# Kernel optimization log

Hardware: AMD Instinct MI355X
Metric: run time of the kernel (lower is better)

The kernel has to match this reference:

```python
import jax, jax.numpy as jnp
import numpy as np

ASSIGN_RATIO = 0.1  # hard-coded inside coarsen_graph in the original
EPS_CUT = 1e-7
EPS_NORM = 1e-12  # torch F.normalize eps


def _normalize_batch_adj(adj):
    # adj: [B, N, N]
    n = adj.shape[1]
    A = adj + jnp.eye(n, dtype=adj.dtype)
    deg_inv_sqrt = jnp.clip(A.sum(-1), 1.0, None) ** -0.5  # [B, N]
    newA = deg_inv_sqrt[..., :, None] * A * deg_inv_sqrt[..., None, :]
    row_mask = (adj.sum(-1) > 0).astype(adj.dtype)  # [B, N]
    return row_mask[..., :, None] * newA


def setup_inputs():
    key = jax.random.key(0)
    k0, k1, k2, k3, k4 = jax.random.split(key, 5)
    B, N, D, T = 512, 128, 256, 512
    concept_hidden = jax.random.normal(k0, (B, N, D), jnp.float32)
    adj = jax.random.uniform(k1, (B, N, N), jnp.float32)
    head = jax.random.randint(k2, (B, T), 0, N)
    lin_w = jax.random.normal(k3, (1, D), jnp.float32) / np.sqrt(D).astype(np.float32)
    bias = jax.random.normal(k4, (1,), jnp.float32)
    return {"concept_hidden": concept_hidden, "adj": adj, "head": head,
            "lin_w": lin_w, "bias": bias}


def reference(concept_hidden, adj, head, lin_w, bias):
    # concept_hidden: [B, N, D], adj: [B, N, N], head: [B, T] node indices
    x = concept_hidden
    B, N, D = x.shape

    out = x @ lin_w.T                      # [B, N, 1]  self.lin(x)
    norm_adj = _normalize_batch_adj(adj)   # [B, N, N]
    out = norm_adj @ out + bias            # [B, N, 1]
    alpha = jax.nn.sigmoid(out ** 2)[..., 0]  # [B, N]

    # batch_num_nodes[i] = len(set(head[i]))  -> count unique via sort
    hs = jnp.sort(head, axis=-1)
    n_uniq = 1 + (hs[:, 1:] != hs[:, :-1]).sum(-1)  # [B]

    # per-sample k = ceil(n * 0.1) + 1 (only when n > 1); cut = k-th largest alpha
    k = jnp.ceil(n_uniq.astype(jnp.float32) * ASSIGN_RATIO).astype(jnp.int32) + 1
    a_desc = jnp.sort(alpha, axis=-1)[:, ::-1]       # descending
    idx = jnp.clip(k - 1, 0, N - 1)
    cut = jnp.take_along_axis(a_desc, idx[:, None], axis=-1)[:, 0]
    cut = jnp.where(n_uniq > 1, cut, jnp.zeros_like(cut))  # [B]

    cut_alpha = jax.nn.relu(alpha + EPS_CUT - cut[:, None])  # [B, N]

    # S = norm_adj * cut_alpha broadcast over rows, then L1-normalize rows
    S = norm_adj * cut_alpha[:, None, :]
    S = S / jnp.clip(jnp.abs(S).sum(-1, keepdims=True), EPS_NORM, None)

    St = jnp.swapaxes(S, 1, 2)             # [B, N, N]
    embedding_tensor = St @ x              # S^T x   [B, N, D]
    new_adj = (St @ adj) @ S               # S^T A S [B, N, N]
    return embedding_tensor, new_adj
```

## Files before the change

kernel.cpp:

```cpp
#include <hip/hip_runtime.h>

#define Bsz 512
#define Nn  128
#define Dd  256
#define Tt  512

typedef __attribute__((ext_vector_type(8))) short short8;
typedef __attribute__((ext_vector_type(4))) float f32x4;

__device__ __forceinline__ ushort f2bf(float f) {
    union { float f; unsigned u; } v; v.f = f;
    unsigned r = v.u + 0x7fffu + ((v.u >> 16) & 1u);
    return (ushort)(r >> 16);
}
__device__ __forceinline__ unsigned pk2(float a, float b) {
    return (unsigned)f2bf(a) | ((unsigned)f2bf(b) << 16);
}
__device__ __forceinline__ float bf2f(ushort u) {
    union { unsigned u; float f; } v; v.u = (unsigned)u << 16; return v.f;
}

__global__ __launch_bounds__(1024, 8) void mega(
    const float* __restrict__ x, const float* __restrict__ adj,
    const int* __restrict__ head, const float* __restrict__ lin_w,
    const float* __restrict__ bias,
    float* __restrict__ emb, float* __restrict__ nadj)
{
    const int b = blockIdx.x, t = threadIdx.x;
    __shared__ __align__(16) ushort adjB[Nn][136];
    __shared__ __align__(16) ushort STl[Nn][136];
    __shared__ float ttS[Nn], disS[Nn], maskS[Nn], alphaS[Nn], uS[Nn], rowcS[Nn];
    __shared__ float dotL[Nn];
    __shared__ int   flags[Nn];
    __shared__ int   nuniq;
    __shared__ float cutS;

    const float bias0 = bias[0];
    if (t < Nn) flags[t] = 0;
    if (t == 0) { nuniq = 0; cutS = 0.f; }

    int hv = 0;
    if (t < 512) {
        hv = head[(size_t)b * Tt + t];
        const int dr = t >> 2, dh = t & 3;
        const float4* xr = (const float4*)(x + ((size_t)b * Nn + dr) * Dd + dh * 64);
        const float4* wr = (const float4*)(lin_w + dh * 64);
        float p = 0.f;
#pragma unroll
        for (int i = 0; i < 16; ++i) {
            float4 v = xr[i], w4 = wr[i];
            p += v.x * w4.x + v.y * w4.y + v.z * w4.z + v.w * w4.w;
        }
        p += __shfl_xor(p, 1, 64);
        p += __shfl_xor(p, 2, 64);
        if (dh == 0) dotL[dr] = p;
    } else {
        const int t2 = t - 512;
        const float* adjb = adj + (size_t)b * Nn * Nn;
#pragma unroll
        for (int i = 0; i < 8; ++i) {
            int f = t2 + 512 * i;
            int rr = f >> 5, c = (f & 31) * 4;
            float4 v = *(const float4*)&adjb[(size_t)rr * Nn + c];
            uint2 w2; w2.x = pk2(v.x, v.y); w2.y = pk2(v.z, v.w);
            *(uint2*)&adjB[rr][c] = w2;
        }
    }
    __syncthreads();

    if (t < Tt) flags[hv] = 1;

    const int r = t >> 3, seg = t & 7;
    {
        short8 a0 = *(const short8*)&adjB[r][seg * 16];
        short8 a1 = *(const short8*)&adjB[r][seg * 16 + 8];
        float s = 0.f;
#pragma unroll
        for (int j = 0; j < 8; ++j) s += bf2f((ushort)a0[j]) + bf2f((ushort)a1[j]);
        s += __shfl_xor(s, 1, 64);
        s += __shfl_xor(s, 2, 64);
        s += __shfl_xor(s, 4, 64);
        if (seg == 0) {
            maskS[r] = (s > 0.f) ? 1.f : 0.f;
            float dis = 1.f / sqrtf(fmaxf(s + 1.f, 1.f));
            disS[r] = dis;
            ttS[r]  = dis * dotL[r];
        }
    }
    __syncthreads();

    {
        short8 a0 = *(const short8*)&adjB[r][seg * 16];
        short8 a1 = *(const short8*)&adjB[r][seg * 16 + 8];
        float s = 0.f;
#pragma unroll
        for (int j = 0; j < 8; ++j) {
            s += bf2f((ushort)a0[j]) * ttS[seg * 16 + j];
            s += bf2f((ushort)a1[j]) * ttS[seg * 16 + 8 + j];
        }
        s += __shfl_xor(s, 1, 64);
        s += __shfl_xor(s, 2, 64);
        s += __shfl_xor(s, 4, 64);
        if (seg == 0) {
            float o = maskS[r] * disS[r] * (s + ttS[r]) + bias0;
            alphaS[r] = 1.f / (1.f + expf(-o * o));
            atomicAdd(&nuniq, flags[r]);
        }
    }
    __syncthreads();

    if (t < Nn) {
        int nu = nuniq;
        if (nu > 1) {
            int idx = (int)ceilf((float)nu * 0.1f);
            if (idx > Nn - 1) idx = Nn - 1;
            float an = alphaS[t];
            int cg = 0, ce = 0;
            for (int j = 0; j < Nn; ++j) {
                float aj = alphaS[j];
                cg += (aj > an); ce += (aj == an);
            }
            if (cg <= idx && idx < cg + ce) cutS = an;
        }
    }
    __syncthreads();
    if (t < Nn) uS[t] = fmaxf(alphaS[t] + 1e-7f - cutS, 0.f) * disS[t];
    __syncthreads();

    {
        short8 a0 = *(const short8*)&adjB[r][seg * 16];
        short8 a1 = *(const short8*)&adjB[r][seg * 16 + 8];
        float s = 0.f;
#pragma unroll
        for (int j = 0; j < 8; ++j) {
            s += bf2f((ushort)a0[j]) * uS[seg * 16 + j];
            s += bf2f((ushort)a1[j]) * uS[seg * 16 + 8 + j];
        }
        s += __shfl_xor(s, 1, 64);
        s += __shfl_xor(s, 2, 64);
        s += __shfl_xor(s, 4, 64);
        if (seg == 0) {
            float rsum = maskS[r] * disS[r] * (uS[r] + s);
            rowcS[r]   = maskS[r] * disS[r] / fmaxf(rsum, 1e-12f);
        }
    }
    __syncthreads();

    {
        const int m = t & 127, sl = t >> 7, k0 = sl * 16;
        const float um = uS[m];
        float vv[16];
#pragma unroll
        for (int j = 0; j < 16; ++j) {
            int k = k0 + j;
            vv[j] = rowcS[k] * (bf2f(adjB[k][m]) + ((k == m) ? 1.f : 0.f)) * um;
        }
        uint4 p0, p1;
        p0.x = pk2(vv[0],  vv[1]);  p0.y = pk2(vv[2],  vv[3]);
        p0.z = pk2(vv[4],  vv[5]);  p0.w = pk2(vv[6],  vv[7]);
        p1.x = pk2(vv[8],  vv[9]);  p1.y = pk2(vv[10], vv[11]);
        p1.z = pk2(vv[12], vv[13]); p1.w = pk2(vv[14], vv[15]);
        *(uint4*)&STl[m][k0]     = p0;
        *(uint4*)&STl[m][k0 + 8] = p1;
    }
    __syncthreads();

    const int lane = t & 63, w = t >> 6;
    const int l15 = lane & 15, quad = lane >> 4;
    const int mrow  = (w & 7) * 16;
    const int nhalf = (w >> 3) * 64;
    f32x4 acc[4];

#pragma unroll
    for (int nt = 0; nt < 4; ++nt) acc[nt] = (f32x4){0.f, 0.f, 0.f, 0.f};
#pragma unroll
    for (int k0 = 0; k0 < 128; k0 += 32) {
        short8 a0 = *(const short8*)&adjB[mrow + l15][k0 + quad * 8];
#pragma unroll
        for (int nt = 0; nt < 4; ++nt) {
            short8 bf = *(const short8*)&STl[nhalf + nt * 16 + l15][k0 + quad * 8];
            acc[nt] = __builtin_amdgcn_mfma_f32_16x16x32_bf16(a0, bf, acc[nt], 0, 0, 0);
        }
    }
    __syncthreads();

    ushort (*PT)[136] = (ushort(*)[136])&adjB[0][0];
#pragma unroll
    for (int nt = 0; nt < 4; ++nt) {
        int j    = nhalf + nt * 16 + l15;
        int mcol = mrow + quad * 4;
        uint2 w2;
        w2.x = pk2(acc[nt][0], acc[nt][1]);
        w2.y = pk2(acc[nt][2], acc[nt][3]);
        *(uint2*)&PT[j][mcol] = w2;
    }
    __syncthreads();

    const int xrow = t & 127, kq0 = t >> 7;
    float xv0[8], xv1[8];
    {
        const float* xb = x + (size_t)b * Nn * Dd + xrow;
#pragma unroll
        for (int k = 0; k < 8; ++k) xv0[k] = xb[(size_t)(8 * kq0 + k) * Dd];
#pragma unroll
        for (int k = 0; k < 8; ++k) xv1[k] = xb[(size_t)(8 * (kq0 + 8) + k) * Dd];
    }

#pragma unroll
    for (int nt = 0; nt < 4; ++nt) acc[nt] = (f32x4){0.f, 0.f, 0.f, 0.f};
#pragma unroll
    for (int k0 = 0; k0 < 128; k0 += 32) {
        short8 a0 = *(const short8*)&STl[mrow + l15][k0 + quad * 8];
#pragma unroll
        for (int nt = 0; nt < 4; ++nt) {
            short8 bf = *(const short8*)&PT[nhalf + nt * 16 + l15][k0 + quad * 8];
            acc[nt] = __builtin_amdgcn_mfma_f32_16x16x32_bf16(a0, bf, acc[nt], 0, 0, 0);
        }
    }
#pragma unroll
    for (int nt = 0; nt < 4; ++nt)
#pragma unroll
        for (int rr2 = 0; rr2 < 4; ++rr2) {
            int row = mrow + quad * 4 + rr2;
            int col = nhalf + nt * 16 + l15;
            nadj[((size_t)b * Nn + row) * Nn + col] = acc[nt][rr2];
        }
    __syncthreads();

    uint (*xTp)[68] = (uint(*)[68])&adjB[0][0];
    const int dcb = (w >> 3) * 64;

    {
        uint4 q;
        q.x = pk2(xv0[0], xv0[1]); q.y = pk2(xv0[2], xv0[3]);
        q.z = pk2(xv0[4], xv0[5]); q.w = pk2(xv0[6], xv0[7]);
        *(uint4*)&xTp[xrow][4 * kq0] = q;
        q.x = pk2(xv1[0], xv1[1]); q.y = pk2(xv1[2], xv1[3]);
        q.z = pk2(xv1[4], xv1[5]); q.w = pk2(xv1[6], xv1[7]);
        *(uint4*)&xTp[xrow][4 * (kq0 + 8)] = q;
    }
    __syncthreads();

    {
        const float* xb = x + (size_t)b * Nn * Dd + 128 + xrow;
#pragma unroll
        for (int k = 0; k < 8; ++k) xv0[k] = xb[(size_t)(8 * kq0 + k) * Dd];
#pragma unroll
        for (int k = 0; k < 8; ++k) xv1[k] = xb[(size_t)(8 * (kq0 + 8) + k) * Dd];
    }

    f32x4 accE[4];
#pragma unroll
    for (int nt = 0; nt < 4; ++nt) accE[nt] = (f32x4){0.f, 0.f, 0.f, 0.f};
#pragma unroll
    for (int ks = 0; ks < 4; ++ks) {
        short8 aE = *(const short8*)&STl[mrow + l15][ks * 32 + quad * 8];
#pragma unroll
        for (int nt = 0; nt < 4; ++nt) {
            short8 bf = *(const short8*)&xTp[dcb + nt * 16 + l15][ks * 16 + quad * 4];
            accE[nt] = __builtin_amdgcn_mfma_f32_16x16x32_bf16(aE, bf, accE[nt], 0, 0, 0);
        }
    }
#pragma unroll
    for (int nt = 0; nt < 4; ++nt)
#pragma unroll
        for (int rr2 = 0; rr2 < 4; ++rr2) {
            int row = mrow + quad * 4 + rr2;
            int col = dcb + nt * 16 + l15;
            emb[((size_t)b * Nn + row) * Dd + col] = accE[nt][rr2];
        }
    __syncthreads();

    {
        uint4 q;
        q.x = pk2(xv0[0], xv0[1]); q.y = pk2(xv0[2], xv0[3]);
        q.z = pk2(xv0[4], xv0[5]); q.w = pk2(xv0[6], xv0[7]);
        *(uint4*)&xTp[xrow][4 * kq0] = q;
        q.x = pk2(xv1[0], xv1[1]); q.y = pk2(xv1[2], xv1[3]);
        q.z = pk2(xv1[4], xv1[5]); q.w = pk2(xv1[6], xv1[7]);
        *(uint4*)&xTp[xrow][4 * (kq0 + 8)] = q;
    }
    __syncthreads();

#pragma unroll
    for (int nt = 0; nt < 4; ++nt) accE[nt] = (f32x4){0.f, 0.f, 0.f, 0.f};
#pragma unroll
    for (int ks = 0; ks < 4; ++ks) {
        short8 aE = *(const short8*)&STl[mrow + l15][ks * 32 + quad * 8];
#pragma unroll
        for (int nt = 0; nt < 4; ++nt) {
            short8 bf = *(const short8*)&xTp[dcb + nt * 16 + l15][ks * 16 + quad * 4];
            accE[nt] = __builtin_amdgcn_mfma_f32_16x16x32_bf16(aE, bf, accE[nt], 0, 0, 0);
        }
    }
#pragma unroll
    for (int nt = 0; nt < 4; ++nt)
#pragma unroll
        for (int rr2 = 0; rr2 < 4; ++rr2) {
            int row = mrow + quad * 4 + rr2;
            int col = 128 + dcb + nt * 16 + l15;
            emb[((size_t)b * Nn + row) * Dd + col] = accE[nt][rr2];
        }
}

extern "C" void kernel_launch(void* const* d_in, const int* in_sizes, int n_in,
                              void* d_out, int out_size, void* d_ws, size_t ws_size,
                              hipStream_t stream)
{
    const float* x     = (const float*)d_in[0];
    const float* adj   = (const float*)d_in[1];
    const int*   head  = (const int*)d_in[2];
    const float* lin_w = (const float*)d_in[3];
    const float* bias  = (const float*)d_in[4];

    float* emb  = (float*)d_out;
    float* nadj = emb + (size_t)Bsz * Nn * Dd;

    mega<<<Bsz, 1024, 0, stream>>>(x, adj, head, lin_w, bias, emb, nadj);
}
```

Baseline: 198.9 us.

## Process two batches per block and prefetch next batch's adj and x-projection

Each block now handles two consecutive batch items. While the first item's matmuls run, it prefetches the second item's adjacency into registers and computes the second item's x·w dot products, so those global loads overlap with compute. The cut-value search is also spread across all threads with shuffle reductions instead of 128 threads each scanning serially. The trade-offs are half as many blocks, which means fewer waves and less parallelism across CUs, and higher register pressure from the prefetch buffers.

```diff
diff --git a/kernel.cpp b/kernel.cpp
--- a/kernel.cpp
+++ b/kernel.cpp
@@ -19,288 +19,331 @@
 __device__ __forceinline__ float bf2f(ushort u) {
     union { unsigned u; float f; } v; v.u = (unsigned)u << 16; return v.f;
 }
-
-__global__ __launch_bounds__(1024, 8) void mega(
+__device__ __forceinline__ float dot4(float4 a, float4 b) {
+    return a.x * b.x + a.y * b.y + a.z * b.z + a.w * b.w;
+}
+
+#define RED(p, off) { float v_ = (p); \
+    v_ += __shfl_xor(v_, 1);  v_ += __shfl_xor(v_, 2);  v_ += __shfl_xor(v_, 4); \
+    v_ += __shfl_xor(v_, 8);  v_ += __shfl_xor(v_, 16); v_ += __shfl_xor(v_, 32); \
+    if (lane == 0) dotL[w + (off)] = v_; }
+
+__global__ __launch_bounds__(1024, 4) void mega(
     const float* __restrict__ x, const float* __restrict__ adj,
     const int* __restrict__ head, const float* __restrict__ lin_w,
     const float* __restrict__ bias,
     float* __restrict__ emb, float* __restrict__ nadj)
 {
-    const int b = blockIdx.x, t = threadIdx.x;
+    const int t = threadIdx.x;
     __shared__ __align__(16) ushort adjB[Nn][136];
     __shared__ __align__(16) ushort STl[Nn][136];
-    __shared__ float ttS[Nn], disS[Nn], maskS[Nn], alphaS[Nn], uS[Nn], rowcS[Nn];
-    __shared__ float dotL[Nn];
+    __shared__ float ttS[Nn], disS[Nn], maskS[Nn], alphaS[Nn], uS[Nn], rowcS[Nn], dotL[Nn];
     __shared__ int   flags[Nn];
     __shared__ int   nuniq;
     __shared__ float cutS;
 
     const float bias0 = bias[0];
-    if (t < Nn) flags[t] = 0;
-    if (t == 0) { nuniq = 0; cutS = 0.f; }
-
-    int hv = 0;
-    if (t < 512) {
-        hv = head[(size_t)b * Tt + t];
-        const int dr = t >> 2, dh = t & 3;
-        const float4* xr = (const float4*)(x + ((size_t)b * Nn + dr) * Dd + dh * 64);
-        const float4* wr = (const float4*)(lin_w + dh * 64);
-        float p = 0.f;
-#pragma unroll
-        for (int i = 0; i < 16; ++i) {
-            float4 v = xr[i], w4 = wr[i];
-            p += v.x * w4.x + v.y * w4.y + v.z * w4.z + v.w * w4.w;
-        }
-        p += __shfl_xor(p, 1, 64);
-        p += __shfl_xor(p, 2, 64);
-        if (dh == 0) dotL[dr] = p;
-    } else {
-        const int t2 = t - 512;
-        const float* adjb = adj + (size_t)b * Nn * Nn;
-#pragma unroll
-        for (int i = 0; i < 8; ++i) {
-            int f = t2 + 512 * i;
-            int rr = f >> 5, c = (f & 31) * 4;
-            float4 v = *(const float4*)&adjb[(size_t)rr * Nn + c];
-            uint2 w2; w2.x = pk2(v.x, v.y); w2.y = pk2(v.z, v.w);
-            *(uint2*)&adjB[rr][c] = w2;
-        }
-    }
-    __syncthreads();
-
-    if (t < Tt) flags[hv] = 1;
-
-    const int r = t >> 3, seg = t & 7;
-    {
-        short8 a0 = *(const short8*)&adjB[r][seg * 16];
-        short8 a1 = *(const short8*)&adjB[r][seg * 16 + 8];
-        float s = 0.f;
-#pragma unroll
-        for (int j = 0; j < 8; ++j) s += bf2f((ushort)a0[j]) + bf2f((ushort)a1[j]);
-        s += __shfl_xor(s, 1, 64);
-        s += __shfl_xor(s, 2, 64);
-        s += __shfl_xor(s, 4, 64);
-        if (seg == 0) {
-            maskS[r] = (s > 0.f) ? 1.f : 0.f;
-            float dis = 1.f / sqrtf(fmaxf(s + 1.f, 1.f));
-            disS[r] = dis;
-            ttS[r]  = dis * dotL[r];
-        }
-    }
-    __syncthreads();
-
-    {
-        short8 a0 = *(const short8*)&adjB[r][seg * 16];
-        short8 a1 = *(const short8*)&adjB[r][seg * 16 + 8];
-        float s = 0.f;
-#pragma unroll
-        for (int j = 0; j < 8; ++j) {
-            s += bf2f((ushort)a0[j]) * ttS[seg * 16 + j];
-            s += bf2f((ushort)a1[j]) * ttS[seg * 16 + 8 + j];
-        }
-        s += __shfl_xor(s, 1, 64);
-        s += __shfl_xor(s, 2, 64);
-        s += __shfl_xor(s, 4, 64);
-        if (seg == 0) {
-            float o = maskS[r] * disS[r] * (s + ttS[r]) + bias0;
-            alphaS[r] = 1.f / (1.f + expf(-o * o));
-            atomicAdd(&nuniq, flags[r]);
-        }
-    }
-    __syncthreads();
-
-    if (t < Nn) {
-        int nu = nuniq;
-        if (nu > 1) {
-            int idx = (int)ceilf((float)nu * 0.1f);
-            if (idx > Nn - 1) idx = Nn - 1;
-            float an = alphaS[t];
-            int cg = 0, ce = 0;
-            for (int j = 0; j < Nn; ++j) {
-                float aj = alphaS[j];
-                cg += (aj > an); ce += (aj == an);
-            }
-            if (cg <= idx && idx < cg + ce) cutS = an;
-        }
-    }
-    __syncthreads();
-    if (t < Nn) uS[t] = fmaxf(alphaS[t] + 1e-7f - cutS, 0.f) * disS[t];
-    __syncthreads();
-
-    {
-        short8 a0 = *(const short8*)&adjB[r][seg * 16];
-        short8 a1 = *(const short8*)&adjB[r][seg * 16 + 8];
-        float s = 0.f;
-#pragma unroll
-        for (int j = 0; j < 8; ++j) {
-            s += bf2f((ushort)a0[j]) * uS[seg * 16 + j];
-            s += bf2f((ushort)a1[j]) * uS[seg * 16 + 8 + j];
-        }
-        s += __shfl_xor(s, 1, 64);
-        s += __shfl_xor(s, 2, 64);
-        s += __shfl_xor(s, 4, 64);
-        if (seg == 0) {
-            float rsum = maskS[r] * disS[r] * (uS[r] + s);
-            rowcS[r]   = maskS[r] * disS[r] / fmaxf(rsum, 1e-12f);
-        }
-    }
-    __syncthreads();
-
-    {
-        const int m = t & 127, sl = t >> 7, k0 = sl * 16;
-        const float um = uS[m];
-        float vv[16];
-#pragma unroll
-        for (int j = 0; j < 16; ++j) {
-            int k = k0 + j;
-            vv[j] = rowcS[k] * (bf2f(adjB[k][m]) + ((k == m) ? 1.f : 0.f)) * um;
-        }
-        uint4 p0, p1;
-        p0.x = pk2(vv[0],  vv[1]);  p0.y = pk2(vv[2],  vv[3]);
-        p0.z = pk2(vv[4],  vv[5]);  p0.w = pk2(vv[6],  vv[7]);
-        p1.x = pk2(vv[8],  vv[9]);  p1.y = pk2(vv[10], vv[11]);
-        p1.z = pk2(vv[12], vv[13]); p1.w = pk2(vv[14], vv[15]);
-        *(uint4*)&STl[m][k0]     = p0;
-        *(uint4*)&STl[m][k0 + 8] = p1;
-    }
-    __syncthreads();
-
     const int lane = t & 63, w = t >> 6;
     const int l15 = lane & 15, quad = lane >> 4;
     const int mrow  = (w & 7) * 16;
     const int nhalf = (w >> 3) * 64;
-    f32x4 acc[4];
-
-#pragma unroll
-    for (int nt = 0; nt < 4; ++nt) acc[nt] = (f32x4){0.f, 0.f, 0.f, 0.f};
-#pragma unroll
-    for (int k0 = 0; k0 < 128; k0 += 32) {
-        short8 a0 = *(const short8*)&adjB[mrow + l15][k0 + quad * 8];
+    const int r = t >> 3, seg = t & 7;
+    const int xrow = t & 127, kq0 = t >> 7;
+
+    float4 pf0 = {0,0,0,0}, pf1 = {0,0,0,0}, pf2 = {0,0,0,0}, pf3 = {0,0,0,0};
+
+    for (int it = 0; it < 2; ++it) {
+        const int b = 2 * blockIdx.x + it;
+
+        if (t < Nn) flags[t] = 0;
+        if (t == 0) { nuniq = 0; cutS = 0.f; }
+
+        int hv = 0;
+        if (t < Tt) hv = head[(size_t)b * Tt + t];
+
+        if (it == 0) {
+            if (t < 512) {
+                const int dr = t >> 2, dh = t & 3;
+                const float4* xr = (const float4*)(x + ((size_t)b * Nn + dr) * Dd + dh * 64);
+                const float4* wr = (const float4*)(lin_w + dh * 64);
+                float p = 0.f;
+#pragma unroll
+                for (int i = 0; i < 16; ++i) p += dot4(xr[i], wr[i]);
+                p += __shfl_xor(p, 1);
+                p += __shfl_xor(p, 2);
+                if (dh == 0) dotL[dr] = p;
+            } else {
+                const int t2 = t - 512;
+                const float* adjb = adj + (size_t)b * Nn * Nn;
+#pragma unroll
+                for (int i = 0; i < 8; ++i) {
+                    int f = t2 + 512 * i;
+                    int rr2 = f >> 5, c = (f & 31) * 4;
+                    float4 v = *(const float4*)&adjb[(size_t)rr2 * Nn + c];
+                    uint2 w2; w2.x = pk2(v.x, v.y); w2.y = pk2(v.z, v.w);
+                    *(uint2*)&adjB[rr2][c] = w2;
+                }
+            }
+        } else {
+            float4 v; int f, rr2, c; uint2 w2;
+            v = pf0; f = t;        rr2 = f >> 5; c = (f & 31) * 4; w2.x = pk2(v.x, v.y); w2.y = pk2(v.z, v.w); *(uint2*)&adjB[rr2][c] = w2;
+            v = pf1; f = t + 1024; rr2 = f >> 5; c = (f & 31) * 4; w2.x = pk2(v.x, v.y); w2.y = pk2(v.z, v.w); *(uint2*)&adjB[rr2][c] = w2;
+            v = pf2; f = t + 2048; rr2 = f >> 5; c = (f & 31) * 4; w2.x = pk2(v.x, v.y); w2.y = pk2(v.z, v.w); *(uint2*)&adjB[rr2][c] = w2;
+            v = pf3; f = t + 3072; rr2 = f >> 5; c = (f & 31) * 4; w2.x = pk2(v.x, v.y); w2.y = pk2(v.z, v.w); *(uint2*)&adjB[rr2][c] = w2;
+        }
+        __syncthreads();
+
+        if (t < Tt) flags[hv] = 1;
+
+        {
+            short8 a0 = *(const short8*)&adjB[r][seg * 16];
+            short8 a1 = *(const short8*)&adjB[r][seg * 16 + 8];
+            float s = 0.f;
+#pragma unroll
+            for (int j = 0; j < 8; ++j) s += bf2f((ushort)a0[j]) + bf2f((ushort)a1[j]);
+            s += __shfl_xor(s, 1); s += __shfl_xor(s, 2); s += __shfl_xor(s, 4);
+            if (seg == 0) {
+                maskS[r] = (s > 0.f) ? 1.f : 0.f;
+                float dis = 1.f / sqrtf(fmaxf(s + 1.f, 1.f));
+                disS[r] = dis;
+                ttS[r]  = dis * dotL[r];
+            }
+        }
+        __syncthreads();
+
+        {
+            short8 a0 = *(const short8*)&adjB[r][seg * 16];
+            short8 a1 = *(const short8*)&adjB[r][seg * 16 + 8];
+            float s = 0.f;
+#pragma unroll
+            for (int j = 0; j < 8; ++j) {
+                s += bf2f((ushort)a0[j]) * ttS[seg * 16 + j];
+                s += bf2f((ushort)a1[j]) * ttS[seg * 16 + 8 + j];
+            }
+            s += __shfl_xor(s, 1); s += __shfl_xor(s, 2); s += __shfl_xor(s, 4);
+            if (seg == 0) {
+                float o = maskS[r] * disS[r] * (s + ttS[r]) + bias0;
+                alphaS[r] = 1.f / (1.f + expf(-o * o));
+                atomicAdd(&nuniq, flags[r]);
+            }
+        }
+        __syncthreads();
+
+        {
+            int nu = nuniq;
+            if (nu > 1) {
+                float an = alphaS[r];
+                int cg = 0, ce = 0;
+                const int j0 = seg * 16;
+#pragma unroll
+                for (int j = 0; j < 16; ++j) {
+                    float aj = alphaS[j0 + j];
+                    cg += (aj > an); ce += (aj == an);
+                }
+                cg += __shfl_xor(cg, 1); cg += __shfl_xor(cg, 2); cg += __shfl_xor(cg, 4);
+                ce += __shfl_xor(ce, 1); ce += __shfl_xor(ce, 2); ce += __shfl_xor(ce, 4);
+                if (seg == 0) {
+                    int idx = (int)ceilf((float)nu * 0.1f);
+                    if (idx > Nn - 1) idx = Nn - 1;
+                    if (cg <= idx && idx < cg + ce) cutS = an;
+                }
+            }
+        }
+        __syncthreads();
+        if (t < Nn) uS[t] = fmaxf(alphaS[t] + 1e-7f - cutS, 0.f) * disS[t];
+        __syncthreads();
+
+        {
+            short8 a0 = *(const short8*)&adjB[r][seg * 16];
+            short8 a1 = *(const short8*)&adjB[r][seg * 16 + 8];
+            float s = 0.f;
+#pragma unroll
+            for (int j = 0; j < 8; ++j) {
+                s += bf2f((ushort)a0[j]) * uS[seg * 16 + j];
+                s += bf2f((ushort)a1[j]) * uS[seg * 16 + 8 + j];
+            }
+            s += __shfl_xor(s, 1); s += __shfl_xor(s, 2); s += __shfl_xor(s, 4);
+            if (seg == 0) {
+                float rsum = maskS[r] * disS[r] * (uS[r] + s);
+                rowcS[r]   = maskS[r] * disS[r] / fmaxf(rsum, 1e-12f);
+            }
+        }
+        __syncthreads();
+
+        {
+            const int m = t & 127, sl = t >> 7, k0 = sl * 16;
+            const float um = uS[m];
+            float vv[16];
+#pragma unroll
+            for (int j = 0; j < 16; ++j) {
+                int k = k0 + j;
+                vv[j] = rowcS[k] * (bf2f(adjB[k][m]) + ((k == m) ? 1.f : 0.f)) * um;
+            }
+            uint4 p0, p1;
+            p0.x = pk2(vv[0],  vv[1]);  p0.y = pk2(vv[2],  vv[3]);
+            p0.z = pk2(vv[4],  vv[5]);  p0.w = pk2(vv[6],  vv[7]);
+            p1.x = pk2(vv[8],  vv[9]);  p1.y = pk2(vv[10], vv[11]);
+            p1.z = pk2(vv[12], vv[13]); p1.w = pk2(vv[14], vv[15]);
+            *(uint4*)&STl[m][k0]     = p0;
+            *(uint4*)&STl[m][k0 + 8] = p1;
+        }
+        __syncthreads();
+
+        if (it == 0) {
+            const float4* a1 = (const float4*)(adj + (size_t)(b + 1) * Nn * Nn);
+            pf0 = a1[t]; pf1 = a1[t + 1024]; pf2 = a1[t + 2048]; pf3 = a1[t + 3072];
+        }
+
+        f32x4 acc[4];
+#pragma unroll
+        for (int nt = 0; nt < 4; ++nt) acc[nt] = (f32x4){0.f, 0.f, 0.f, 0.f};
+#pragma unroll
+        for (int k0 = 0; k0 < 128; k0 += 32) {
+            short8 a0 = *(const short8*)&adjB[mrow + l15][k0 + quad * 8];
+#pragma unroll
+            for (int nt = 0; nt < 4; ++nt) {
+                short8 bf = *(const short8*)&STl[nhalf + nt * 16 + l15][k0 + quad * 8];
+                acc[nt] = __builtin_amdgcn_mfma_f32_16x16x32_bf16(a0, bf, acc[nt], 0, 0, 0);
+            }
+        }
+        __syncthreads();
+
+        ushort (*PT)[136] = (ushort(*)[136])&adjB[0][0];
 #pragma unroll
         for (int nt = 0; nt < 4; ++nt) {
-            short8 bf = *(const short8*)&STl[nhalf + nt * 16 + l15][k0 + quad * 8];
-            acc[nt] = __builtin_amdgcn_mfma_f32_16x16x32_bf16(a0, bf, acc[nt], 0, 0, 0);
+            int j    = nhalf + nt * 16 + l15;
+            int mcol = mrow + quad * 4;
+            uint2 w2;
+            w2.x = pk2(acc[nt][0], acc[nt][1]);
+            w2.y = pk2(acc[nt][2], acc[nt][3]);
+            *(uint2*)&PT[j][mcol] = w2;
+        }
+        __syncthreads();
+
+#pragma unroll
+        for (int nt = 0; nt < 4; ++nt) acc[nt] = (f32x4){0.f, 0.f, 0.f, 0.f};
+#pragma unroll
+        for (int k0 = 0; k0 < 128; k0 += 32) {
+            short8 a0 = *(const short8*)&STl[mrow + l15][k0 + quad * 8];
+#pragma unroll
+            for (int nt = 0; nt < 4; ++nt) {
+                short8 bf = *(const short8*)&PT[nhalf + nt * 16 + l15][k0 + quad * 8];
+                acc[nt] = __builtin_amdgcn_mfma_f32_16x16x32_bf16(a0, bf, acc[nt], 0, 0, 0);
+            }
+        }
+#pragma unroll
+        for (int nt = 0; nt < 4; ++nt)
+#pragma unroll
+            for (int rr2 = 0; rr2 < 4; ++rr2) {
+                int row = mrow + quad * 4 + rr2;
+                int col = nhalf + nt * 16 + l15;
+                nadj[((size_t)b * Nn + row) * Nn + col] = acc[nt][rr2];
+            }
+        __syncthreads();
+
+        uint (*xTp)[68] = (uint(*)[68])&adjB[0][0];
+        const int dcb = (w >> 3) * 64;
+        const float4* xf1 = (const float4*)(x + (size_t)(b + 1) * Nn * Dd);
+        float4 wv = ((const float4*)lin_w)[lane];
+        float4 qa0 = {0,0,0,0}, qa1 = {0,0,0,0}, qa2 = {0,0,0,0}, qa3 = {0,0,0,0};
+        float pA0 = 0.f, pA1 = 0.f, pA2 = 0.f, pA3 = 0.f;
+        float pB0 = 0.f, pB1 = 0.f, pB2 = 0.f, pB3 = 0.f;
+
+        if (it == 0) {
+            qa0 = xf1[t]; qa1 = xf1[t + 1024]; qa2 = xf1[t + 2048]; qa3 = xf1[t + 3072];
+        }
+
+        {
+            const float* xb = x + (size_t)b * Nn * Dd + xrow;
+            float e[8], g[8];
+#pragma unroll
+            for (int k = 0; k < 8; ++k) e[k] = xb[(size_t)(8 * kq0 + k) * Dd];
+#pragma unroll
+            for (int k = 0; k < 8; ++k) g[k] = xb[(size_t)(8 * (kq0 + 8) + k) * Dd];
+            uint4 q;
+            q.x = pk2(e[0], e[1]); q.y = pk2(e[2], e[3]);
+            q.z = pk2(e[4], e[5]); q.w = pk2(e[6], e[7]);
+            *(uint4*)&xTp[xrow][4 * kq0] = q;
+            q.x = pk2(g[0], g[1]); q.y = pk2(g[2], g[3]);
+            q.z = pk2(g[4], g[5]); q.w = pk2(g[6], g[7]);
+            *(uint4*)&xTp[xrow][4 * (kq0 + 8)] = q;
+        }
+        __syncthreads();
+
+        f32x4 accE[4];
+#pragma unroll
+        for (int nt = 0; nt < 4; ++nt) accE[nt] = (f32x4){0.f, 0.f, 0.f, 0.f};
+#pragma unroll
+        for (int ks = 0; ks < 4; ++ks) {
+            short8 aE = *(const short8*)&STl[mrow + l15][ks * 32 + quad * 8];
+#pragma unroll
+            for (int nt = 0; nt < 4; ++nt) {
+                short8 bf = *(const short8*)&xTp[dcb + nt * 16 + l15][ks * 16 + quad * 4];
+                accE[nt] = __builtin_amdgcn_mfma_f32_16x16x32_bf16(aE, bf, accE[nt], 0, 0, 0);
+            }
+        }
+#pragma unroll
+        for (int nt = 0; nt < 4; ++nt)
+#pragma unroll
+            for (int rr2 = 0; rr2 < 4; ++rr2) {
+                int row = mrow + quad * 4 + rr2;
+                int col = dcb + nt * 16 + l15;
+                emb[((size_t)b * Nn + row) * Dd + col] = accE[nt][rr2];
+            }
+        __syncthreads();
+
+        if (it == 0) {
+            pA0 = dot4(qa0, wv); pA1 = dot4(qa1, wv);
+            pA2 = dot4(qa2, wv); pA3 = dot4(qa3, wv);
+            qa0 = xf1[t + 4096]; qa1 = xf1[t + 5120];
+            qa2 = xf1[t + 6144]; qa3 = xf1[t + 7168];
+        }
+
+        {
+            const float* xb = x + (size_t)b * Nn * Dd + 128 + xrow;
+            float e[8], g[8];
+#pragma unroll
+            for (int k = 0; k < 8; ++k) e[k] = xb[(size_t)(8 * kq0 + k) * Dd];
+#pragma unroll
+            for (int k = 0; k < 8; ++k) g[k] = xb[(size_t)(8 * (kq0 + 8) + k) * Dd];
+            uint4 q;
+            q.x = pk2(e[0], e[1]); q.y = pk2(e[2], e[3]);
+            q.z = pk2(e[4], e[5]); q.w = pk2(e[6], e[7]);
+            *(uint4*)&xTp[xrow][4 * kq0] = q;
+            q.x = pk2(g[0], g[1]); q.y = pk2(g[2], g[3]);
+            q.z = pk2(g[4], g[5]); q.w = pk2(g[6], g[7]);
+            *(uint4*)&xTp[xrow][4 * (kq0 + 8)] = q;
+        }
+        __syncthreads();
+
+#pragma unroll
+        for (int nt = 0; nt < 4; ++nt) accE[nt] = (f32x4){0.f, 0.f, 0.f, 0.f};
+#pragma unroll
+        for (int ks = 0; ks < 4; ++ks) {
+            short8 aE = *(const short8*)&STl[mrow + l15][ks * 32 + quad * 8];
+#pragma unroll
+            for (int nt = 0; nt < 4; ++nt) {
+                short8 bf = *(const short8*)&xTp[dcb + nt * 16 + l15][ks * 16 + quad * 4];
+                accE[nt] = __builtin_amdgcn_mfma_f32_16x16x32_bf16(aE, bf, accE[nt], 0, 0, 0);
+            }
+        }
+#pragma unroll
+        for (int nt = 0; nt < 4; ++nt)
+#pragma unroll
+            for (int rr2 = 0; rr2 < 4; ++rr2) {
+                int row = mrow + quad * 4 + rr2;
+                int col = 128 + dcb + nt * 16 + l15;
+                emb[((size_t)b * Nn + row) * Dd + col] = accE[nt][rr2];
+            }
+
+        if (it == 0) {
+            pB0 = dot4(qa0, wv); pB1 = dot4(qa1, wv);
+            pB2 = dot4(qa2, wv); pB3 = dot4(qa3, wv);
+            RED(pA0, 0)  RED(pA1, 16) RED(pA2, 32) RED(pA3, 48)
+            RED(pB0, 64) RED(pB1, 80) RED(pB2, 96) RED(pB3, 112)
+            __syncthreads();
         }
     }
-    __syncthreads();
-
-    ushort (*PT)[136] = (ushort(*)[136])&adjB[0][0];
-#pragma unroll
-    for (int nt = 0; nt < 4; ++nt) {
-        int j    = nhalf + nt * 16 + l15;
-        int mcol = mrow + quad * 4;
-        uint2 w2;
-        w2.x = pk2(acc[nt][0], acc[nt][1]);
-        w2.y = pk2(acc[nt][2], acc[nt][3]);
-        *(uint2*)&PT[j][mcol] = w2;
-    }
-    __syncthreads();
-
-    const int xrow = t & 127, kq0 = t >> 7;
-    float xv0[8], xv1[8];
-    {
-        const float* xb = x + (size_t)b * Nn * Dd + xrow;
-#pragma unroll
-        for (int k = 0; k < 8; ++k) xv0[k] = xb[(size_t)(8 * kq0 + k) * Dd];
-#pragma unroll
-        for (int k = 0; k < 8; ++k) xv1[k] = xb[(size_t)(8 * (kq0 + 8) + k) * Dd];
-    }
-
-#pragma unroll
-    for (int nt = 0; nt < 4; ++nt) acc[nt] = (f32x4){0.f, 0.f, 0.f, 0.f};
-#pragma unroll
-    for (int k0 = 0; k0 < 128; k0 += 32) {
-        short8 a0 = *(const short8*)&STl[mrow + l15][k0 + quad * 8];
-#pragma unroll
-        for (int nt = 0; nt < 4; ++nt) {
-            short8 bf = *(const short8*)&PT[nhalf + nt * 16 + l15][k0 + quad * 8];
-            acc[nt] = __builtin_amdgcn_mfma_f32_16x16x32_bf16(a0, bf, acc[nt], 0, 0, 0);
-        }
-    }
-#pragma unroll
-    for (int nt = 0; nt < 4; ++nt)
-#pragma unroll
-        for (int rr2 = 0; rr2 < 4; ++rr2) {
-            int row = mrow + quad * 4 + rr2;
-            int col = nhalf + nt * 16 + l15;
-            nadj[((size_t)b * Nn + row) * Nn + col] = acc[nt][rr2];
-        }
-    __syncthreads();
-
-    uint (*xTp)[68] = (uint(*)[68])&adjB[0][0];
-    const int dcb = (w >> 3) * 64;
-
-    {
-        uint4 q;
-        q.x = pk2(xv0[0], xv0[1]); q.y = pk2(xv0[2], xv0[3]);
-        q.z = pk2(xv0[4], xv0[5]); q.w = pk2(xv0[6], xv0[7]);
-        *(uint4*)&xTp[xrow][4 * kq0] = q;
-        q.x = pk2(xv1[0], xv1[1]); q.y = pk2(xv1[2], xv1[3]);
-        q.z = pk2(xv1[4], xv1[5]); q.w = pk2(xv1[6], xv1[7]);
-        *(uint4*)&xTp[xrow][4 * (kq0 + 8)] = q;
-    }
-    __syncthreads();
-
-    {
-        const float* xb = x + (size_t)b * Nn * Dd + 128 + xrow;
-#pragma unroll
-        for (int k = 0; k < 8; ++k) xv0[k] = xb[(size_t)(8 * kq0 + k) * Dd];
-#pragma unroll
-        for (int k = 0; k < 8; ++k) xv1[k] = xb[(size_t)(8 * (kq0 + 8) + k) * Dd];
-    }
-
-    f32x4 accE[4];
-#pragma unroll
-    for (int nt = 0; nt < 4; ++nt) accE[nt] = (f32x4){0.f, 0.f, 0.f, 0.f};
-#pragma unroll
-    for (int ks = 0; ks < 4; ++ks) {
-        short8 aE = *(const short8*)&STl[mrow + l15][ks * 32 + quad * 8];
-#pragma unroll
-        for (int nt = 0; nt < 4; ++nt) {
-            short8 bf = *(const short8*)&xTp[dcb + nt * 16 + l15][ks * 16 + quad * 4];
-            accE[nt] = __builtin_amdgcn_mfma_f32_16x16x32_bf16(aE, bf, accE[nt], 0, 0, 0);
-        }
-    }
-#pragma unroll
-    for (int nt = 0; nt < 4; ++nt)
-#pragma unroll
-        for (int rr2 = 0; rr2 < 4; ++rr2) {
-            int row = mrow + quad * 4 + rr2;
-            int col = dcb + nt * 16 + l15;
-            emb[((size_t)b * Nn + row) * Dd + col] = accE[nt][rr2];
-        }
-    __syncthreads();
-
-    {
-        uint4 q;
-        q.x = pk2(xv0[0], xv0[1]); q.y = pk2(xv0[2], xv0[3]);
-        q.z = pk2(xv0[4], xv0[5]); q.w = pk2(xv0[6], xv0[7]);
-        *(uint4*)&xTp[xrow][4 * kq0] = q;
-        q.x = pk2(xv1[0], xv1[1]); q.y = pk2(xv1[2], xv1[3]);
-        q.z = pk2(xv1[4], xv1[5]); q.w = pk2(xv1[6], xv1[7]);
-        *(uint4*)&xTp[xrow][4 * (kq0 + 8)] = q;
-    }
-    __syncthreads();
-
-#pragma unroll
-    for (int nt = 0; nt < 4; ++nt) accE[nt] = (f32x4){0.f, 0.f, 0.f, 0.f};
-#pragma unroll
-    for (int ks = 0; ks < 4; ++ks) {
-        short8 aE = *(const short8*)&STl[mrow + l15][ks * 32 + quad * 8];
-#pragma unroll
-        for (int nt = 0; nt < 4; ++nt) {
-            short8 bf = *(const short8*)&xTp[dcb + nt * 16 + l15][ks * 16 + quad * 4];
-            accE[nt] = __builtin_amdgcn_mfma_f32_16x16x32_bf16(aE, bf, accE[nt], 0, 0, 0);
-        }
-    }
-#pragma unroll
-    for (int nt = 0; nt < 4; ++nt)
-#pragma unroll
-        for (int rr2 = 0; rr2 < 4; ++rr2) {
-            int row = mrow + quad * 4 + rr2;
-            int col = 128 + dcb + nt * 16 + l15;
-            emb[((size_t)b * Nn + row) * Dd + col] = accE[nt][rr2];
-        }
 }
 
 extern "C" void kernel_launch(void* const* d_in, const int* in_sizes, int n_in,
@@ -316,5 +359,5 @@
     float* emb  = (float*)d_out;
     float* nadj = emb + (size_t)Bsz * Nn * Dd;
 
-    mega<<<Bsz, 1024, 0, stream>>>(x, adj, head, lin_w, bias, emb, nadj);
-}
+    mega<<<Bsz / 2, 1024, 0, stream>>>(x, adj, head, lin_w, bias, emb, nadj);
+}
```

Result: slower. 250.1 us (+25.8%).

## Load all of x and adj up front, staging transposed x in dedicated LDS

Applied to the files above, without the earlier changes.

All global loads of x, adj and head are issued at kernel start. The lin_w dot product is computed from the transposed x registers with wave shuffles. The transposed bf16 x is written once into two dedicated LDS buffers, so the later x reloads and their barriers are gone, and the uS array and its barrier are replaced by inline recomputation. The cut search is spread over 8 threads per row. This costs more LDS (about 138KB) and more registers, and the launch bound drops from 8 to 4 waves per EU, which can lower occupancy.

```diff
diff --git a/kernel.cpp b/kernel.cpp
--- a/kernel.cpp
+++ b/kernel.cpp
@@ -20,17 +20,19 @@
     union { unsigned u; float f; } v; v.u = (unsigned)u << 16; return v.f;
 }
 
-__global__ __launch_bounds__(1024, 8) void mega(
+__global__ __launch_bounds__(1024, 4) void mega(
     const float* __restrict__ x, const float* __restrict__ adj,
     const int* __restrict__ head, const float* __restrict__ lin_w,
     const float* __restrict__ bias,
     float* __restrict__ emb, float* __restrict__ nadj)
 {
-    const int b = blockIdx.x, t = threadIdx.x;
+    const int t = threadIdx.x, b = blockIdx.x;
     __shared__ __align__(16) ushort adjB[Nn][136];
     __shared__ __align__(16) ushort STl[Nn][136];
-    __shared__ float ttS[Nn], disS[Nn], maskS[Nn], alphaS[Nn], uS[Nn], rowcS[Nn];
-    __shared__ float dotL[Nn];
+    __shared__ __align__(16) uint   xT0[Nn][68];
+    __shared__ __align__(16) uint   xT1[Nn][68];
+    __shared__ float ttS[Nn], disS[Nn], maskS[Nn], alphaS[Nn], rowcS[Nn];
+    __shared__ float dotP2[Nn][2];
     __shared__ int   flags[Nn];
     __shared__ int   nuniq;
     __shared__ float cutS;
@@ -39,52 +41,87 @@
     if (t < Nn) flags[t] = 0;
     if (t == 0) { nuniq = 0; cutS = 0.f; }
 
+    const int lane = t & 63, w = t >> 6;
+    const int l15 = lane & 15, quad = lane >> 4;
+    const int mrow  = (w & 7) * 16;
+    const int nhalf = (w >> 3) * 64;
+    const int r = t >> 3, seg = t & 7;
+    const int xrow = t & 127, kq0 = t >> 7;
+
     int hv = 0;
-    if (t < 512) {
-        hv = head[(size_t)b * Tt + t];
-        const int dr = t >> 2, dh = t & 3;
-        const float4* xr = (const float4*)(x + ((size_t)b * Nn + dr) * Dd + dh * 64);
-        const float4* wr = (const float4*)(lin_w + dh * 64);
-        float p = 0.f;
-#pragma unroll
-        for (int i = 0; i < 16; ++i) {
-            float4 v = xr[i], w4 = wr[i];
-            p += v.x * w4.x + v.y * w4.y + v.z * w4.z + v.w * w4.w;
-        }
-        p += __shfl_xor(p, 1, 64);
-        p += __shfl_xor(p, 2, 64);
-        if (dh == 0) dotL[dr] = p;
-    } else {
-        const int t2 = t - 512;
-        const float* adjb = adj + (size_t)b * Nn * Nn;
-#pragma unroll
-        for (int i = 0; i < 8; ++i) {
-            int f = t2 + 512 * i;
-            int rr = f >> 5, c = (f & 31) * 4;
-            float4 v = *(const float4*)&adjb[(size_t)rr * Nn + c];
-            uint2 w2; w2.x = pk2(v.x, v.y); w2.y = pk2(v.z, v.w);
-            *(uint2*)&adjB[rr][c] = w2;
-        }
+    if (t < Tt) hv = head[(size_t)b * Tt + t];
+
+    float e0[8], g0[8], e1[8], g1[8];
+    {
+        const float* xb = x + (size_t)b * Nn * Dd + xrow;
+#pragma unroll
+        for (int k = 0; k < 8; ++k) e0[k] = xb[(size_t)(8 * kq0 + k) * Dd];
+#pragma unroll
+        for (int k = 0; k < 8; ++k) g0[k] = xb[(size_t)(64 + 8 * kq0 + k) * Dd];
+#pragma unroll
+        for (int k = 0; k < 8; ++k) e1[k] = xb[(size_t)(8 * kq0 + k) * Dd + 128];
+#pragma unroll
+        for (int k = 0; k < 8; ++k) g1[k] = xb[(size_t)(64 + 8 * kq0 + k) * Dd + 128];
+    }
+    float4 av0, av1, av2, av3;
+    {
+        const float4* adjb = (const float4*)(adj + (size_t)b * Nn * Nn);
+        av0 = adjb[t]; av1 = adjb[t + 1024]; av2 = adjb[t + 2048]; av3 = adjb[t + 3072];
+    }
+    const float wv0 = lin_w[xrow], wv1 = lin_w[128 + xrow];
+
+#pragma unroll
+    for (int k = 0; k < 8; ++k) {
+        float re = e0[k] * wv0 + e1[k] * wv1;
+        float rg = g0[k] * wv0 + g1[k] * wv1;
+        re += __shfl_xor(re, 1); re += __shfl_xor(re, 2); re += __shfl_xor(re, 4);
+        re += __shfl_xor(re, 8); re += __shfl_xor(re, 16); re += __shfl_xor(re, 32);
+        rg += __shfl_xor(rg, 1); rg += __shfl_xor(rg, 2); rg += __shfl_xor(rg, 4);
+        rg += __shfl_xor(rg, 8); rg += __shfl_xor(rg, 16); rg += __shfl_xor(rg, 32);
+        if (lane == 0) {
+            dotP2[8 * kq0 + k][w & 1]      = re;
+            dotP2[64 + 8 * kq0 + k][w & 1] = rg;
+        }
+    }
+
+    {
+        uint4 q;
+        q.x = pk2(e0[0], e0[1]); q.y = pk2(e0[2], e0[3]);
+        q.z = pk2(e0[4], e0[5]); q.w = pk2(e0[6], e0[7]);
+        *(uint4*)&xT0[xrow][4 * kq0] = q;
+        q.x = pk2(g0[0], g0[1]); q.y = pk2(g0[2], g0[3]);
+        q.z = pk2(g0[4], g0[5]); q.w = pk2(g0[6], g0[7]);
+        *(uint4*)&xT0[xrow][4 * (kq0 + 8)] = q;
+        q.x = pk2(e1[0], e1[1]); q.y = pk2(e1[2], e1[3]);
+        q.z = pk2(e1[4], e1[5]); q.w = pk2(e1[6], e1[7]);
+        *(uint4*)&xT1[xrow][4 * kq0] = q;
+        q.x = pk2(g1[0], g1[1]); q.y = pk2(g1[2], g1[3]);
+        q.z = pk2(g1[4], g1[5]); q.w = pk2(g1[6], g1[7]);
+        *(uint4*)&xT1[xrow][4 * (kq0 + 8)] = q;
+    }
+    {
+        float4 v; int f, rr2, c; uint2 w2;
+        v = av0; f = t;        rr2 = f >> 5; c = (f & 31) * 4; w2.x = pk2(v.x, v.y); w2.y = pk2(v.z, v.w); *(uint2*)&adjB[rr2][c] = w2;
+        v = av1; f = t + 1024; rr2 = f >> 5; c = (f & 31) * 4; w2.x = pk2(v.x, v.y); w2.y = pk2(v.z, v.w); *(uint2*)&adjB[rr2][c] = w2;
+        v = av2; f = t + 2048; rr2 = f >> 5; c = (f & 31) * 4; w2.x = pk2(v.x, v.y); w2.y = pk2(v.z, v.w); *(uint2*)&adjB[rr2][c] = w2;
+        v = av3; f = t + 3072; rr2 = f >> 5; c = (f & 31) * 4; w2.x = pk2(v.x, v.y); w2.y = pk2(v.z, v.w); *(uint2*)&adjB[rr2][c] = w2;
     }
     __syncthreads();
 
     if (t < Tt) flags[hv] = 1;
 
-    const int r = t >> 3, seg = t & 7;
     {
         short8 a0 = *(const short8*)&adjB[r][seg * 16];
         short8 a1 = *(const short8*)&adjB[r][seg * 16 + 8];
         float s = 0.f;
 #pragma unroll
         for (int j = 0; j < 8; ++j) s += bf2f((ushort)a0[j]) + bf2f((ushort)a1[j]);
-        s += __shfl_xor(s, 1, 64);
-        s += __shfl_xor(s, 2, 64);
-        s += __shfl_xor(s, 4, 64);
+        s += __shfl_xor(s, 1); s += __shfl_xor(s, 2); s += __shfl_xor(s, 4);
         if (seg == 0) {
             maskS[r] = (s > 0.f) ? 1.f : 0.f;
             float dis = 1.f / sqrtf(fmaxf(s + 1.f, 1.f));
             disS[r] = dis;
-            ttS[r]  = dis * dotL[r];
+            ttS[r]  = dis * (dotP2[r][0] + dotP2[r][1]);
         }
     }
     __syncthreads();
@@ -98,9 +135,7 @@
             s += bf2f((ushort)a0[j]) * ttS[seg * 16 + j];
             s += bf2f((ushort)a1[j]) * ttS[seg * 16 + 8 + j];
         }
-        s += __shfl_xor(s, 1, 64);
-        s += __shfl_xor(s, 2, 64);
-        s += __shfl_xor(s, 4, 64);
+        s += __shfl_xor(s, 1); s += __shfl_xor(s, 2); s += __shfl_xor(s, 4);
         if (seg == 0) {
             float o = maskS[r] * disS[r] * (s + ttS[r]) + bias0;
             alphaS[r] = 1.f / (1.f + expf(-o * o));
@@ -109,46 +144,53 @@
     }
     __syncthreads();
 
-    if (t < Nn) {
+    {
         int nu = nuniq;
         if (nu > 1) {
-            int idx = (int)ceilf((float)nu * 0.1f);
-            if (idx > Nn - 1) idx = Nn - 1;
-            float an = alphaS[t];
+            float an = alphaS[r];
             int cg = 0, ce = 0;
-            for (int j = 0; j < Nn; ++j) {
-                float aj = alphaS[j];
+            const int j0 = seg * 16;
+#pragma unroll
+            for (int j = 0; j < 16; ++j) {
+                float aj = alphaS[j0 + j];
                 cg += (aj > an); ce += (aj == an);
             }
-            if (cg <= idx && idx < cg + ce) cutS = an;
-        }
-    }
-    __syncthreads();
-    if (t < Nn) uS[t] = fmaxf(alphaS[t] + 1e-7f - cutS, 0.f) * disS[t];
-    __syncthreads();
-
-    {
+            cg += __shfl_xor(cg, 1); cg += __shfl_xor(cg, 2); cg += __shfl_xor(cg, 4);
+            ce += __shfl_xor(ce, 1); ce += __shfl_xor(ce, 2); ce += __shfl_xor(ce, 4);
+            if (seg == 0) {
+                int idx = (int)ceilf((float)nu * 0.1f);
+                if (idx > Nn - 1) idx = Nn - 1;
+                if (cg <= idx && idx < cg + ce) cutS = an;
+            }
+        }
+    }
+    __syncthreads();
+
+    {
+        const float cut = cutS;
         short8 a0 = *(const short8*)&adjB[r][seg * 16];
         short8 a1 = *(const short8*)&adjB[r][seg * 16 + 8];
         float s = 0.f;
 #pragma unroll
         for (int j = 0; j < 8; ++j) {
-            s += bf2f((ushort)a0[j]) * uS[seg * 16 + j];
-            s += bf2f((ushort)a1[j]) * uS[seg * 16 + 8 + j];
-        }
-        s += __shfl_xor(s, 1, 64);
-        s += __shfl_xor(s, 2, 64);
-        s += __shfl_xor(s, 4, 64);
+            int j0 = seg * 16 + j, j1 = seg * 16 + 8 + j;
+            float u0 = fmaxf(alphaS[j0] + 1e-7f - cut, 0.f) * disS[j0];
+            float u1 = fmaxf(alphaS[j1] + 1e-7f - cut, 0.f) * disS[j1];
+            s += bf2f((ushort)a0[j]) * u0 + bf2f((ushort)a1[j]) * u1;
+        }
+        s += __shfl_xor(s, 1); s += __shfl_xor(s, 2); s += __shfl_xor(s, 4);
         if (seg == 0) {
-            float rsum = maskS[r] * disS[r] * (uS[r] + s);
+            float ur   = fmaxf(alphaS[r] + 1e-7f - cut, 0.f) * disS[r];
+            float rsum = maskS[r] * disS[r] * (ur + s);
             rowcS[r]   = maskS[r] * disS[r] / fmaxf(rsum, 1e-12f);
         }
     }
     __syncthreads();
 
     {
+        const float cut = cutS;
         const int m = t & 127, sl = t >> 7, k0 = sl * 16;
-        const float um = uS[m];
+        const float um = fmaxf(alphaS[m] + 1e-7f - cut, 0.f) * disS[m];
         float vv[16];
 #pragma unroll
         for (int j = 0; j < 16; ++j) {
@@ -165,12 +207,7 @@
     }
     __syncthreads();
 
-    const int lane = t & 63, w = t >> 6;
-    const int l15 = lane & 15, quad = lane >> 4;
-    const int mrow  = (w & 7) * 16;
-    const int nhalf = (w >> 3) * 64;
     f32x4 acc[4];
-
 #pragma unroll
     for (int nt = 0; nt < 4; ++nt) acc[nt] = (f32x4){0.f, 0.f, 0.f, 0.f};
 #pragma unroll
@@ -196,16 +233,6 @@
     }
     __syncthreads();
 
-    const int xrow = t & 127, kq0 = t >> 7;
-    float xv0[8], xv1[8];
-    {
-        const float* xb = x + (size_t)b * Nn * Dd + xrow;
-#pragma unroll
-        for (int k = 0; k < 8; ++k) xv0[k] = xb[(size_t)(8 * kq0 + k) * Dd];
-#pragma unroll
-        for (int k = 0; k < 8; ++k) xv1[k] = xb[(size_t)(8 * (kq0 + 8) + k) * Dd];
-    }
-
 #pragma unroll
     for (int nt = 0; nt < 4; ++nt) acc[nt] = (f32x4){0.f, 0.f, 0.f, 0.f};
 #pragma unroll
@@ -225,40 +252,22 @@
             int col = nhalf + nt * 16 + l15;
             nadj[((size_t)b * Nn + row) * Nn + col] = acc[nt][rr2];
         }
-    __syncthreads();
-
-    uint (*xTp)[68] = (uint(*)[68])&adjB[0][0];
+
     const int dcb = (w >> 3) * 64;
-
-    {
-        uint4 q;
-        q.x = pk2(xv0[0], xv0[1]); q.y = pk2(xv0[2], xv0[3]);
-        q.z = pk2(xv0[4], xv0[5]); q.w = pk2(xv0[6], xv0[7]);
-        *(uint4*)&xTp[xrow][4 * kq0] = q;
-        q.x = pk2(xv1[0], xv1[1]); q.y = pk2(xv1[2], xv1[3]);
-        q.z = pk2(xv1[4], xv1[5]); q.w = pk2(xv1[6], xv1[7]);
-        *(uint4*)&xTp[xrow][4 * (kq0 + 8)] = q;
-    }
-    __syncthreads();
-
-    {
-        const float* xb = x + (size_t)b * Nn * Dd + 128 + xrow;
-#pragma unroll
-        for (int k = 0; k < 8; ++k) xv0[k] = xb[(size_t)(8 * kq0 + k) * Dd];
-#pragma unroll
-        for (int k = 0; k < 8; ++k) xv1[k] = xb[(size_t)(8 * (kq0 + 8) + k) * Dd];
-    }
+    short8 aE[4];
+#pragma unroll
+    for (int ks = 0; ks < 4; ++ks)
+        aE[ks] = *(const short8*)&STl[mrow + l15][ks * 32 + quad * 8];
 
     f32x4 accE[4];
 #pragma unroll
     for (int nt = 0; nt < 4; ++nt) accE[nt] = (f32x4){0.f, 0.f, 0.f, 0.f};
 #pragma unroll
     for (int ks = 0; ks < 4; ++ks) {
-        short8 aE = *(const short8*)&STl[mrow + l15][ks * 32 + quad * 8];
 #pragma unroll
         for (int nt = 0; nt < 4; ++nt) {
-            short8 bf = *(const short8*)&xTp[dcb + nt * 16 + l15][ks * 16 + quad * 4];
-            accE[nt] = __builtin_amdgcn_mfma_f32_16x16x32_bf16(aE, bf, accE[nt], 0, 0, 0);
+            short8 bf = *(const short8*)&xT0[dcb + nt * 16 + l15][ks * 16 + quad * 4];
+            accE[nt] = __builtin_amdgcn_mfma_f32_16x16x32_bf16(aE[ks], bf, accE[nt], 0, 0, 0);
         }
     }
 #pragma unroll
@@ -269,28 +278,15 @@
             int col = dcb + nt * 16 + l15;
             emb[((size_t)b * Nn + row) * Dd + col] = accE[nt][rr2];
         }
-    __syncthreads();
-
-    {
-        uint4 q;
-        q.x = pk2(xv0[0], xv0[1]); q.y = pk2(xv0[2], xv0[3]);
-        q.z = pk2(xv0[4], xv0[5]); q.w = pk2(xv0[6], xv0[7]);
-        *(uint4*)&xTp[xrow][4 * kq0] = q;
-        q.x = pk2(xv1[0], xv1[1]); q.y = pk2(xv1[2], xv1[3]);
-        q.z = pk2(xv1[4], xv1[5]); q.w = pk2(xv1[6], xv1[7]);
-        *(uint4*)&xTp[xrow][4 * (kq0 + 8)] = q;
-    }
-    __syncthreads();
 
 #pragma unroll
     for (int nt = 0; nt < 4; ++nt) accE[nt] = (f32x4){0.f, 0.f, 0.f, 0.f};
 #pragma unroll
     for (int ks = 0; ks < 4; ++ks) {
-        short8 aE = *(const short8*)&STl[mrow + l15][ks * 32 + quad * 8];
 #pragma unroll
         for (int nt = 0; nt < 4; ++nt) {
-            short8 bf = *(const short8*)&xTp[dcb + nt * 16 + l15][ks * 16 + quad * 4];
-            accE[nt] = __builtin_amdgcn_mfma_f32_16x16x32_bf16(aE, bf, accE[nt], 0, 0, 0);
+            short8 bf = *(const short8*)&xT1[dcb + nt * 16 + l15][ks * 16 + quad * 4];
+            accE[nt] = __builtin_amdgcn_mfma_f32_16x16x32_bf16(aE[ks], bf, accE[nt], 0, 0, 0);
         }
     }
 #pragma unroll
```

Result: no change. 200.1 us (+0.6%).
